# Kernel tuning notes

Measured on AMD Instinct MI355X. Metric: run time of the kernel, lower is better.

Reference implementation:

```python
import jax, jax.numpy as jnp
import numpy as np
from functools import partial

B = 256          # batch_size (== hidden_dim, required by the module's broadcasting)
T = 512          # seq_length
H = 256          # hidden_dim == dim_out
E = 6            # emb_dim
V = 10           # num_input_digits
C = 10           # num_classes


def _kaiming(key, shape):
    fan_in = shape[1]
    return jax.random.normal(key, shape, dtype=jnp.float32) * np.sqrt(2.0 / fan_in)


def setup_inputs() -> dict:
    key = jax.random.key(0)
    ks = jax.random.split(key, 12)
    inp = {
        "x": jax.random.randint(ks[0], (B, T), 0, V),
        "emb": jax.random.normal(ks[1], (V, E), dtype=jnp.float32),
        "Wxg": _kaiming(ks[2], (H, E)), "Whg": _kaiming(ks[3], (H, H)), "bg": jnp.zeros((H,), jnp.float32),
        "Wxi": _kaiming(ks[4], (H, E)), "Whi": _kaiming(ks[5], (H, H)), "bi": jnp.zeros((H,), jnp.float32),
        "Wxf": _kaiming(ks[6], (H, E)), "Whf": _kaiming(ks[7], (H, H)), "bf": jnp.zeros((H,), jnp.float32),
        "Wxo": _kaiming(ks[8], (H, E)), "Who": _kaiming(ks[9], (H, H)), "bo": jnp.zeros((H,), jnp.float32),
        "Wp": _kaiming(ks[10], (C, H)), "bp": jnp.zeros((C,), jnp.float32),
    }
    return inp


def reference(x, emb, Wxg, Whg, bg, Wxi, Whi, bi, Wxf, Whf, bf, Wxo, Who, bo, Wp, bp):
    # x: (B, T) int -> embed -> (B, T, E)
    xe = emb[x]
    # time-major (T, E, B): each step uses x_t.T as in the torch code
    xt_seq = jnp.transpose(xe, (1, 2, 0))

    h0 = jnp.zeros((H, B), jnp.float32)  # h lives as (H, B) per original math
    c0 = jnp.zeros((H, B), jnp.float32)

    def step(carry, xTt):  # xTt: (E, B)
        h, c = carry
        # NOTE: bias (H,) broadcasts over the trailing batch axis (H==B), faithful
        # to the original torch broadcasting.
        g = jnp.tanh(Wxg @ xTt + Whg @ h + bg)
        i = jax.nn.sigmoid(Wxi @ xTt + Whi @ h + bi)
        f = jax.nn.sigmoid(Wxf @ xTt + Whf @ h + bf)
        o = jax.nn.sigmoid(Wxo @ xTt + Who @ h + bo)
        c = g * i + c * f
        h = jnp.tanh(c) * o
        return (h, c), None

    (h, c), _ = jax.lax.scan(step, (h0, c0), xt_seq)
    return (Wp @ h).T + bp  # (B, C)
```

## Files before the change

### kernel.cpp

```cpp
#include <hip/hip_runtime.h>
#include <hip/hip_bf16.h>


typedef __attribute__((ext_vector_type(4))) int   int4v;
typedef __attribute__((ext_vector_type(4))) float float4v;

#define MFMA_I8(a, b, c) __builtin_amdgcn_mfma_i32_16x16x64_i8(a, b, c, 0, 0, 0)

#define K_TANH (-2.8853900817779268f)
#define K_SIG  (-1.4426950408889634f)

#define HSTRIDE 320

__device__ __forceinline__ short f2b(float f) {
    __hip_bfloat16 b = __float2bfloat16(f); return *(short*)&b;
}
__device__ __forceinline__ float b2f(short s) {
    union { unsigned int u; float f; } v; v.u = ((unsigned int)(unsigned short)s) << 16; return v.f;
}
__device__ __forceinline__ float fexp2(float x) {
#if __has_builtin(__builtin_amdgcn_exp2f)
    return __builtin_amdgcn_exp2f(x);
#else
    return __expf(x * 0.6931471805599453f);
#endif
}
__device__ __forceinline__ float frcp(float x) { return __builtin_amdgcn_rcpf(x); }

__global__ __attribute__((amdgpu_flat_work_group_size(1024, 1024), amdgpu_waves_per_eu(4, 4)))
void lstm_i8(
    const int* __restrict__ x,
    const float* __restrict__ emb,
    const float* __restrict__ Wxg, const float* __restrict__ Whg, const float* __restrict__ bg,
    const float* __restrict__ Wxi, const float* __restrict__ Whi, const float* __restrict__ bi,
    const float* __restrict__ Wxf, const float* __restrict__ Whf, const float* __restrict__ bff,
    const float* __restrict__ Wxo, const float* __restrict__ Who, const float* __restrict__ bo,
    const float* __restrict__ Wp, const float* __restrict__ bp,
    float* __restrict__ out)
{
    const int tid = threadIdx.x, bid = blockIdx.x;
    const int c0 = bid * 2;
    const int w = tid >> 6, lane = tid & 63;
    const int l = lane & 15, q = lane >> 4;
    const int col = l & 1;
    const int si  = (l >> 1) & 3;
    const int dup = (l >> 3) & 1;
    const int rw  = 16 * w;
    const int row = rw + 4 * q + si;

    __shared__ __align__(16) unsigned int hbuf[2][2 * HSTRIDE / 4];
    __shared__ __align__(16) short hfin[2 * 264];
    __shared__ unsigned char xdig2[512 * 2];
    __shared__ __align__(16) float tblC[2 * 10 * 1024];
    __shared__ float scaleL[4 * 256];

    const float* WxT[4] = {Wxg, Wxi, Wxf, Wxo};
    const float* WhT[4] = {Whg, Whi, Whf, Who};
    const float* bT[4]  = {bg, bi, bff, bo};

    if (tid < 2 * HSTRIDE / 4) hbuf[0][tid] = 0u;
    if (tid < 1024)
        xdig2[tid] = (unsigned char)x[(c0 + (tid & 1)) * 512 + (tid >> 1)];

    for (int i = tid; i < 5120; i += 1024) {
        int cc  = i / 2560;
        int rem = i - cc * 2560;
        int d = rem >> 8, r = rem & 255;
        float4v v;
        #pragma unroll
        for (int g = 0; g < 4; g++) {
            float s = 0.f;
            #pragma unroll
            for (int e = 0; e < 6; e++) s += WxT[g][r * 6 + e] * emb[d * 6 + e];
            v[g] = (s + bT[g][c0 + cc]) * (g == 0 ? K_TANH : K_SIG);
        }
        *(float4v*)&tblC[cc * 10240 + d * 1024 + r * 4] = v;
    }

    int4v wa[4][4];
    #pragma unroll
    for (int g = 0; g < 4; g++) {
        const float* Wr = WhT[g] + (rw + l) * 256 + q * 16;
        float mx = 0.f;
        #pragma unroll
        for (int kt = 0; kt < 4; kt++)
            #pragma unroll
            for (int c4 = 0; c4 < 4; c4++) {
                float4v v = *(const float4v*)(Wr + kt * 64 + c4 * 4);
                #pragma unroll
                for (int j = 0; j < 4; j++) mx = fmaxf(mx, fabsf(v[j]));
            }
        mx = fmaxf(mx, __shfl_xor(mx, 16));
        mx = fmaxf(mx, __shfl_xor(mx, 32));
        mx = fmaxf(mx, 1e-20f);
        if (q == 0) scaleL[g * 256 + rw + l] = mx;
        float qs = 127.f / mx;
        #pragma unroll
        for (int kt = 0; kt < 4; kt++) {
            int4v f;
            #pragma unroll
            for (int dw = 0; dw < 4; dw++) {
                float4v v = *(const float4v*)(Wr + kt * 64 + dw * 4);
                int word = 0;
                #pragma unroll
                for (int byt = 0; byt < 4; byt++) {
                    int z = (int)rintf(v[byt] * qs);
                    word |= (z & 255) << (8 * byt);
                }
                f[dw] = word;
            }
            wa[g][kt] = f;
        }
    }

    __syncthreads();

    float dscl[4];
    #pragma unroll
    for (int g = 0; g < 4; g++) {
        float kk = (g == 0 ? K_TANH : K_SIG) * (1.f / 16129.f);
        dscl[g] = scaleL[g * 256 + row] * kk;
    }

    const bool bi1 = (si & 1) != 0;
    const bool bi2 = (si & 2) != 0;
    const float* tprow = tblC + col * 10240 + row * 4;
    const int hoff = col * HSTRIDE + row;

    float cs = 0.f, hl = 0.f;

    for (int t = 0; t < 512; t++) {
        const int p = t & 1;
        const char* hbase = (const char*)hbuf[p] + col * HSTRIDE + q * 16;

        int dg = xdig2[t * 2 + col];
        float4v tb = *(const float4v*)(tprow + dg * 1024);

        int4v a0e = {0,0,0,0}, a0o = {0,0,0,0};
        int4v a1e = {0,0,0,0}, a1o = {0,0,0,0};
        int4v a2  = {0,0,0,0}, a3  = {0,0,0,0};
        int4v hf0 = *(const int4v*)(hbase + 0 * 64);
        int4v hf1 = *(const int4v*)(hbase + 1 * 64);
        int4v hf2 = *(const int4v*)(hbase + 2 * 64);
        int4v hf3 = *(const int4v*)(hbase + 3 * 64);
        a0e = MFMA_I8(wa[0][0], hf0, a0e); a0o = MFMA_I8(wa[0][1], hf1, a0o);
        a1e = MFMA_I8(wa[1][0], hf0, a1e); a1o = MFMA_I8(wa[1][1], hf1, a1o);
        a2  = MFMA_I8(wa[2][0], hf0, a2);  a2  = MFMA_I8(wa[2][1], hf1, a2);
        a3  = MFMA_I8(wa[3][0], hf0, a3);  a3  = MFMA_I8(wa[3][1], hf1, a3);
        a0e = MFMA_I8(wa[0][2], hf2, a0e); a0o = MFMA_I8(wa[0][3], hf3, a0o);
        a1e = MFMA_I8(wa[1][2], hf2, a1e); a1o = MFMA_I8(wa[1][3], hf3, a1o);
        a2  = MFMA_I8(wa[2][2], hf2, a2);  a2  = MFMA_I8(wa[2][3], hf3, a2);
        a3  = MFMA_I8(wa[3][2], hf2, a3);  a3  = MFMA_I8(wa[3][3], hf3, a3);
        int4v acc0, acc1;
        #pragma unroll
        for (int i = 0; i < 4; i++) { acc0[i] = a0e[i] + a0o[i]; acc1[i] = a1e[i] + a1o[i]; }

        int av0, av1, av2, av3;
        { int s0 = bi1 ? acc0[1] : acc0[0]; int s1 = bi1 ? acc0[3] : acc0[2]; av0 = bi2 ? s1 : s0; }
        { int s0 = bi1 ? acc1[1] : acc1[0]; int s1 = bi1 ? acc1[3] : acc1[2]; av1 = bi2 ? s1 : s0; }
        { int s0 = bi1 ? a2[1]   : a2[0];   int s1 = bi1 ? a2[3]   : a2[2];   av2 = bi2 ? s1 : s0; }
        { int s0 = bi1 ? a3[1]   : a3[0];   int s1 = bi1 ? a3[3]   : a3[2];   av3 = bi2 ? s1 : s0; }
        {
            float pg = fmaf((float)av0, dscl[0], tb[0]);
            float pi = fmaf((float)av1, dscl[1], tb[1]);
            float pf = fmaf((float)av2, dscl[2], tb[2]);
            float po = fmaf((float)av3, dscl[3], tb[3]);
            float Eg = fexp2(pg), Ei = fexp2(pi), Ef = fexp2(pf), Eo = fexp2(po);
            float m1  = (1.f + Eg) * (1.f + Ei);
            float fp1 = 1.f + Ef;
            float num = fmaf(cs, m1, (1.f - Eg) * fp1);
            float c   = num * frcp(m1 * fp1);
            cs = c;
            float Ec = fexp2(K_TANH * c);
            float hh = (1.f - Ec) * frcp((1.f + Ec) * (1.f + Eo));
            hl = hh;
            if (dup == 0)
                *((char*)hbuf[1 - p] + hoff) = (char)((int)rintf(hh * 127.f));
        }
        __syncthreads();
    }

    if (dup == 0) hfin[col * 264 + row] = f2b(hl);
    __syncthreads();

    if (tid < 20) {
        int pc = tid / 10, cls = tid - pc * 10;
        const short* hcol = &hfin[pc * 264];
        const float* wrow = Wp + cls * 256;
        float s = 0.f;
        #pragma unroll 8
        for (int k = 0; k < 256; k++) s += b2f(hcol[k]) * wrow[k];
        out[(c0 + pc) * 10 + cls] = s + bp[cls];
    }
}

extern "C" void kernel_launch(void* const* d_in, const int* in_sizes, int n_in,
                              void* d_out, int out_size, void* d_ws, size_t ws_size,
                              hipStream_t stream) {
    const int*   x   = (const int*)d_in[0];
    const float* emb = (const float*)d_in[1];
    const float* Wxg = (const float*)d_in[2];
    const float* Whg = (const float*)d_in[3];
    const float* bg  = (const float*)d_in[4];
    const float* Wxi = (const float*)d_in[5];
    const float* Whi = (const float*)d_in[6];
    const float* bi  = (const float*)d_in[7];
    const float* Wxf = (const float*)d_in[8];
    const float* Whf = (const float*)d_in[9];
    const float* bff = (const float*)d_in[10];
    const float* Wxo = (const float*)d_in[11];
    const float* Who = (const float*)d_in[12];
    const float* bo  = (const float*)d_in[13];
    const float* Wp  = (const float*)d_in[14];
    const float* bp  = (const float*)d_in[15];

    hipLaunchKernelGGL(lstm_i8, dim3(128), dim3(1024), 0, stream,
                       x, emb, Wxg, Whg, bg, Wxi, Whi, bi, Wxf, Whf, bff,
                       Wxo, Who, bo, Wp, bp, (float*)d_out);
}
```

Measured before the change: 553.9 us.

## Replace per-step block barrier with LDS flag counters per wave group

The per-timestep __syncthreads is replaced by four shared-memory counters, one per group of four waves. Each group bumps its counter with a workgroup-scope release atomic after writing its slice of h. Each wave waits only on the counter for the h chunk it is about to read, and consumes the four chunks in a rotated order so it starts with data from a different group. MFMA bursts are also wrapped in s_setprio to raise wave priority. This aims to cut barrier stall and let waves overlap across steps, at the cost of spin-polling on volatile LDS and a more delicate ordering argument for reuse of the double buffer.

```diff
diff --git a/kernel.cpp b/kernel.cpp
--- a/kernel.cpp
+++ b/kernel.cpp
@@ -26,6 +26,11 @@
 #endif
 }
 __device__ __forceinline__ float frcp(float x) { return __builtin_amdgcn_rcpf(x); }
+
+__device__ __forceinline__ void spin_ge(volatile int* f, int target) {
+    if (__builtin_expect(*f >= target, 1)) return;
+    while (*f < target) __builtin_amdgcn_s_sleep(1);
+}
 
 __global__ __attribute__((amdgpu_flat_work_group_size(1024, 1024), amdgpu_waves_per_eu(4, 4)))
 void lstm_i8(
@@ -41,6 +46,7 @@
     const int tid = threadIdx.x, bid = blockIdx.x;
     const int c0 = bid * 2;
     const int w = tid >> 6, lane = tid & 63;
+    const int jg = w >> 2;
     const int l = lane & 15, q = lane >> 4;
     const int col = l & 1;
     const int si  = (l >> 1) & 3;
@@ -53,6 +59,7 @@
     __shared__ unsigned char xdig2[512 * 2];
     __shared__ __align__(16) float tblC[2 * 10 * 1024];
     __shared__ float scaleL[4 * 256];
+    __shared__ int wcnt[4];
 
     const float* WxT[4] = {Wxg, Wxi, Wxf, Wxo};
     const float* WhT[4] = {Whg, Whi, Whf, Who};
@@ -61,6 +68,7 @@
     if (tid < 2 * HSTRIDE / 4) hbuf[0][tid] = 0u;
     if (tid < 1024)
         xdig2[tid] = (unsigned char)x[(c0 + (tid & 1)) * 512 + (tid >> 1)];
+    if (tid < 4) wcnt[tid] = 0;
 
     for (int i = tid; i < 5120; i += 1024) {
         int cc  = i / 2560;
@@ -77,7 +85,7 @@
         *(float4v*)&tblC[cc * 10240 + d * 1024 + r * 4] = v;
     }
 
-    int4v wa[4][4];
+    int4v wb[4][4];
     #pragma unroll
     for (int g = 0; g < 4; g++) {
         const float* Wr = WhT[g] + (rw + l) * 256 + q * 16;
@@ -88,7 +96,7 @@
             for (int c4 = 0; c4 < 4; c4++) {
                 float4v v = *(const float4v*)(Wr + kt * 64 + c4 * 4);
                 #pragma unroll
-                for (int j = 0; j < 4; j++) mx = fmaxf(mx, fabsf(v[j]));
+                for (int jj = 0; jj < 4; jj++) mx = fmaxf(mx, fabsf(v[jj]));
             }
         mx = fmaxf(mx, __shfl_xor(mx, 16));
         mx = fmaxf(mx, __shfl_xor(mx, 32));
@@ -96,8 +104,9 @@
         if (q == 0) scaleL[g * 256 + rw + l] = mx;
         float qs = 127.f / mx;
         #pragma unroll
-        for (int kt = 0; kt < 4; kt++) {
-            int4v f;
+        for (int kk = 0; kk < 4; kk++) {
+            const int kt = (jg + 1 + kk) & 3;
+            int4v fr;
             #pragma unroll
             for (int dw = 0; dw < 4; dw++) {
                 float4v v = *(const float4v*)(Wr + kt * 64 + dw * 4);
@@ -107,9 +116,9 @@
                     int z = (int)rintf(v[byt] * qs);
                     word |= (z & 255) << (8 * byt);
                 }
-                f[dw] = word;
+                fr[dw] = word;
             }
-            wa[g][kt] = f;
+            wb[g][kk] = fr;
         }
     }
 
@@ -127,10 +136,18 @@
     const float* tprow = tblC + col * 10240 + row * 4;
     const int hoff = col * HSTRIDE + row;
 
+    const int kts0 = (jg + 1) & 3, kts1 = (jg + 2) & 3, kts2 = (jg + 3) & 3, kts3 = jg;
+    volatile int* fl0 = (volatile int*)&wcnt[kts0];
+    volatile int* fl1 = (volatile int*)&wcnt[kts1];
+    volatile int* fl2 = (volatile int*)&wcnt[kts2];
+    volatile int* fl3 = (volatile int*)&wcnt[kts3];
+    const int ho0 = kts0 * 64, ho1 = kts1 * 64, ho2 = kts2 * 64, ho3 = kts3 * 64;
+
     float cs = 0.f, hl = 0.f;
 
     for (int t = 0; t < 512; t++) {
         const int p = t & 1;
+        const int tt = t << 2;
         const char* hbase = (const char*)hbuf[p] + col * HSTRIDE + q * 16;
 
         int dg = xdig2[t * 2 + col];
@@ -139,18 +156,52 @@
         int4v a0e = {0,0,0,0}, a0o = {0,0,0,0};
         int4v a1e = {0,0,0,0}, a1o = {0,0,0,0};
         int4v a2  = {0,0,0,0}, a3  = {0,0,0,0};
-        int4v hf0 = *(const int4v*)(hbase + 0 * 64);
-        int4v hf1 = *(const int4v*)(hbase + 1 * 64);
-        int4v hf2 = *(const int4v*)(hbase + 2 * 64);
-        int4v hf3 = *(const int4v*)(hbase + 3 * 64);
-        a0e = MFMA_I8(wa[0][0], hf0, a0e); a0o = MFMA_I8(wa[0][1], hf1, a0o);
-        a1e = MFMA_I8(wa[1][0], hf0, a1e); a1o = MFMA_I8(wa[1][1], hf1, a1o);
-        a2  = MFMA_I8(wa[2][0], hf0, a2);  a2  = MFMA_I8(wa[2][1], hf1, a2);
-        a3  = MFMA_I8(wa[3][0], hf0, a3);  a3  = MFMA_I8(wa[3][1], hf1, a3);
-        a0e = MFMA_I8(wa[0][2], hf2, a0e); a0o = MFMA_I8(wa[0][3], hf3, a0o);
-        a1e = MFMA_I8(wa[1][2], hf2, a1e); a1o = MFMA_I8(wa[1][3], hf3, a1o);
-        a2  = MFMA_I8(wa[2][2], hf2, a2);  a2  = MFMA_I8(wa[2][3], hf3, a2);
-        a3  = MFMA_I8(wa[3][2], hf2, a3);  a3  = MFMA_I8(wa[3][3], hf3, a3);
+
+        if (t) spin_ge(fl0, tt);
+        asm volatile("" ::: "memory");
+        {
+            int4v hf = *(const int4v*)(hbase + ho0);
+            __builtin_amdgcn_s_setprio(1);
+            a0e = MFMA_I8(wb[0][0], hf, a0e);
+            a1e = MFMA_I8(wb[1][0], hf, a1e);
+            a2  = MFMA_I8(wb[2][0], hf, a2);
+            a3  = MFMA_I8(wb[3][0], hf, a3);
+            __builtin_amdgcn_s_setprio(0);
+        }
+        if (t) spin_ge(fl1, tt);
+        asm volatile("" ::: "memory");
+        {
+            int4v hf = *(const int4v*)(hbase + ho1);
+            __builtin_amdgcn_s_setprio(1);
+            a0o = MFMA_I8(wb[0][1], hf, a0o);
+            a1o = MFMA_I8(wb[1][1], hf, a1o);
+            a2  = MFMA_I8(wb[2][1], hf, a2);
+            a3  = MFMA_I8(wb[3][1], hf, a3);
+            __builtin_amdgcn_s_setprio(0);
+        }
+        if (t) spin_ge(fl2, tt);
+        asm volatile("" ::: "memory");
+        {
+            int4v hf = *(const int4v*)(hbase + ho2);
+            __builtin_amdgcn_s_setprio(1);
+            a0e = MFMA_I8(wb[0][2], hf, a0e);
+            a1e = MFMA_I8(wb[1][2], hf, a1e);
+            a2  = MFMA_I8(wb[2][2], hf, a2);
+            a3  = MFMA_I8(wb[3][2], hf, a3);
+            __builtin_amdgcn_s_setprio(0);
+        }
+        if (t) spin_ge(fl3, tt);
+        asm volatile("" ::: "memory");
+        {
+            int4v hf = *(const int4v*)(hbase + ho3);
+            __builtin_amdgcn_s_setprio(1);
+            a0o = MFMA_I8(wb[0][3], hf, a0o);
+            a1o = MFMA_I8(wb[1][3], hf, a1o);
+            a2  = MFMA_I8(wb[2][3], hf, a2);
+            a3  = MFMA_I8(wb[3][3], hf, a3);
+            __builtin_amdgcn_s_setprio(0);
+        }
+
         int4v acc0, acc1;
         #pragma unroll
         for (int i = 0; i < 4; i++) { acc0[i] = a0e[i] + a0o[i]; acc1[i] = a1e[i] + a1o[i]; }
@@ -174,10 +225,13 @@
             float Ec = fexp2(K_TANH * c);
             float hh = (1.f - Ec) * frcp((1.f + Ec) * (1.f + Eo));
             hl = hh;
+            if (t == 0 && jg != 0) spin_ge((volatile int*)&wcnt[jg - 1], 4);
             if (dup == 0)
                 *((char*)hbuf[1 - p] + hoff) = (char)((int)rintf(hh * 127.f));
         }
-        __syncthreads();
+        asm volatile("" ::: "memory");
+        if (lane == 0)
+            __hip_atomic_fetch_add(&wcnt[jg], 1, __ATOMIC_RELEASE, __HIP_MEMORY_SCOPE_WORKGROUP);
     }
 
     if (dup == 0) hfin[col * 264 + row] = f2b(hl);
```

New measurement: 698.0 us. +26.0%, slower.

## Halve block to 512 threads with two row tiles per wave and pipelined gate math

Applied to the files above, without the earlier changes.

The block shrinks from 1024 to 512 threads. Each wave now owns two 16-row tiles, so it keeps twice the int8 weight fragments in registers, and the duplicate lanes that previously did redundant work are removed. Inside each timestep, the gate activations for each gate run as soon as that gate's MFMAs finish, and the next step's bias-table lookup is prefetched using precomputed byte offsets. The loop is unrolled by two to fix the ping-pong buffers, and even waves get higher priority. Fewer waves should make each barrier cheaper, at the cost of a longer serial MFMA chain per wave and more register pressure.

```diff
diff --git a/kernel.cpp b/kernel.cpp
--- a/kernel.cpp
+++ b/kernel.cpp
@@ -27,7 +27,7 @@
 }
 __device__ __forceinline__ float frcp(float x) { return __builtin_amdgcn_rcpf(x); }
 
-__global__ __attribute__((amdgpu_flat_work_group_size(1024, 1024), amdgpu_waves_per_eu(4, 4)))
+__global__ __attribute__((amdgpu_flat_work_group_size(512, 512), amdgpu_waves_per_eu(2, 2)))
 void lstm_i8(
     const int* __restrict__ x,
     const float* __restrict__ emb,
@@ -42,15 +42,15 @@
     const int c0 = bid * 2;
     const int w = tid >> 6, lane = tid & 63;
     const int l = lane & 15, q = lane >> 4;
-    const int col = l & 1;
-    const int si  = (l >> 1) & 3;
-    const int dup = (l >> 3) & 1;
-    const int rw  = 16 * w;
-    const int row = rw + 4 * q + si;
+    const int col = lane & 1;
+    const int rtb = (lane >> 1) & 1;
+    const int si  = (lane >> 2) & 3;
+    const int rwb = 32 * w;
+    const int row = rwb + 16 * rtb + 4 * q + si;
 
     __shared__ __align__(16) unsigned int hbuf[2][2 * HSTRIDE / 4];
     __shared__ __align__(16) short hfin[2 * 264];
-    __shared__ unsigned char xdig2[512 * 2];
+    __shared__ __align__(4) unsigned short xoff[2][512];
     __shared__ __align__(16) float tblC[2 * 10 * 1024];
     __shared__ float scaleL[4 * 256];
 
@@ -59,10 +59,12 @@
     const float* bT[4]  = {bg, bi, bff, bo};
 
     if (tid < 2 * HSTRIDE / 4) hbuf[0][tid] = 0u;
-    if (tid < 1024)
-        xdig2[tid] = (unsigned char)x[(c0 + (tid & 1)) * 512 + (tid >> 1)];
-
-    for (int i = tid; i < 5120; i += 1024) {
+    for (int i = tid; i < 1024; i += 512) {
+        int cc = i >> 9, t = i & 511;
+        xoff[cc][t] = (unsigned short)(x[(c0 + cc) * 512 + t] << 12);
+    }
+
+    for (int i = tid; i < 5120; i += 512) {
         int cc  = i / 2560;
         int rem = i - cc * 2560;
         int d = rem >> 8, r = rem & 255;
@@ -77,43 +79,48 @@
         *(float4v*)&tblC[cc * 10240 + d * 1024 + r * 4] = v;
     }
 
-    int4v wa[4][4];
+    int4v wa[2][4][4];
     #pragma unroll
-    for (int g = 0; g < 4; g++) {
-        const float* Wr = WhT[g] + (rw + l) * 256 + q * 16;
-        float mx = 0.f;
+    for (int rt = 0; rt < 2; rt++) {
         #pragma unroll
-        for (int kt = 0; kt < 4; kt++)
+        for (int g = 0; g < 4; g++) {
+            const float* Wr = WhT[g] + (rwb + rt * 16 + l) * 256 + q * 16;
+            float mx = 0.f;
             #pragma unroll
-            for (int c4 = 0; c4 < 4; c4++) {
-                float4v v = *(const float4v*)(Wr + kt * 64 + c4 * 4);
+            for (int kt = 0; kt < 4; kt++)
                 #pragma unroll
-                for (int j = 0; j < 4; j++) mx = fmaxf(mx, fabsf(v[j]));
+                for (int c4 = 0; c4 < 4; c4++) {
+                    float4v v = *(const float4v*)(Wr + kt * 64 + c4 * 4);
+                    #pragma unroll
+                    for (int j = 0; j < 4; j++) mx = fmaxf(mx, fabsf(v[j]));
+                }
+            mx = fmaxf(mx, __shfl_xor(mx, 16));
+            mx = fmaxf(mx, __shfl_xor(mx, 32));
+            mx = fmaxf(mx, 1e-20f);
+            if (q == 0) scaleL[g * 256 + rwb + rt * 16 + l] = mx;
+            float qs = 127.f / mx;
+            #pragma unroll
+            for (int kt = 0; kt < 4; kt++) {
+                int4v f;
+                #pragma unroll
+                for (int dw = 0; dw < 4; dw++) {
+                    float4v v = *(const float4v*)(Wr + kt * 64 + dw * 4);
+                    int word = 0;
+                    #pragma unroll
+                    for (int byt = 0; byt < 4; byt++) {
+                        int z = (int)rintf(v[byt] * qs);
+                        word |= (z & 255) << (8 * byt);
+                    }
+                    f[dw] = word;
+                }
+                wa[rt][g][kt] = f;
             }
-        mx = fmaxf(mx, __shfl_xor(mx, 16));
-        mx = fmaxf(mx, __shfl_xor(mx, 32));
-        mx = fmaxf(mx, 1e-20f);
-        if (q == 0) scaleL[g * 256 + rw + l] = mx;
-        float qs = 127.f / mx;
-        #pragma unroll
-        for (int kt = 0; kt < 4; kt++) {
-            int4v f;
-            #pragma unroll
-            for (int dw = 0; dw < 4; dw++) {
-                float4v v = *(const float4v*)(Wr + kt * 64 + dw * 4);
-                int word = 0;
-                #pragma unroll
-                for (int byt = 0; byt < 4; byt++) {
-                    int z = (int)rintf(v[byt] * qs);
-                    word |= (z & 255) << (8 * byt);
-                }
-                f[dw] = word;
-            }
-            wa[g][kt] = f;
         }
     }
 
     __syncthreads();
+
+    if ((w & 1) == 0) __builtin_amdgcn_s_setprio(1);
 
     float dscl[4];
     #pragma unroll
@@ -124,63 +131,114 @@
 
     const bool bi1 = (si & 1) != 0;
     const bool bi2 = (si & 2) != 0;
-    const float* tprow = tblC + col * 10240 + row * 4;
+    const bool brt = rtb != 0;
+    const char* tprowB = (const char*)(tblC + col * 10240 + row * 4);
     const int hoff = col * HSTRIDE + row;
 
+    const char* hb0 = (const char*)hbuf[0] + col * HSTRIDE + q * 16;
+    const char* hb1 = (const char*)hbuf[1] + col * HSTRIDE + q * 16;
+    char* hw0 = (char*)hbuf[0] + hoff;
+    char* hw1 = (char*)hbuf[1] + hoff;
+    const char* xobase = (const char*)&xoff[col][0];
+
+    const int4v Z = {0, 0, 0, 0};
+
     float cs = 0.f, hl = 0.f;
 
-    for (int t = 0; t < 512; t++) {
-        const int p = t & 1;
-        const char* hbase = (const char*)hbuf[p] + col * HSTRIDE + q * 16;
-
-        int dg = xdig2[t * 2 + col];
-        float4v tb = *(const float4v*)(tprow + dg * 1024);
-
-        int4v a0e = {0,0,0,0}, a0o = {0,0,0,0};
-        int4v a1e = {0,0,0,0}, a1o = {0,0,0,0};
-        int4v a2  = {0,0,0,0}, a3  = {0,0,0,0};
-        int4v hf0 = *(const int4v*)(hbase + 0 * 64);
-        int4v hf1 = *(const int4v*)(hbase + 1 * 64);
-        int4v hf2 = *(const int4v*)(hbase + 2 * 64);
-        int4v hf3 = *(const int4v*)(hbase + 3 * 64);
-        a0e = MFMA_I8(wa[0][0], hf0, a0e); a0o = MFMA_I8(wa[0][1], hf1, a0o);
-        a1e = MFMA_I8(wa[1][0], hf0, a1e); a1o = MFMA_I8(wa[1][1], hf1, a1o);
-        a2  = MFMA_I8(wa[2][0], hf0, a2);  a2  = MFMA_I8(wa[2][1], hf1, a2);
-        a3  = MFMA_I8(wa[3][0], hf0, a3);  a3  = MFMA_I8(wa[3][1], hf1, a3);
-        a0e = MFMA_I8(wa[0][2], hf2, a0e); a0o = MFMA_I8(wa[0][3], hf3, a0o);
-        a1e = MFMA_I8(wa[1][2], hf2, a1e); a1o = MFMA_I8(wa[1][3], hf3, a1o);
-        a2  = MFMA_I8(wa[2][2], hf2, a2);  a2  = MFMA_I8(wa[2][3], hf3, a2);
-        a3  = MFMA_I8(wa[3][2], hf2, a3);  a3  = MFMA_I8(wa[3][3], hf3, a3);
-        int4v acc0, acc1;
-        #pragma unroll
-        for (int i = 0; i < 4; i++) { acc0[i] = a0e[i] + a0o[i]; acc1[i] = a1e[i] + a1o[i]; }
-
-        int av0, av1, av2, av3;
-        { int s0 = bi1 ? acc0[1] : acc0[0]; int s1 = bi1 ? acc0[3] : acc0[2]; av0 = bi2 ? s1 : s0; }
-        { int s0 = bi1 ? acc1[1] : acc1[0]; int s1 = bi1 ? acc1[3] : acc1[2]; av1 = bi2 ? s1 : s0; }
-        { int s0 = bi1 ? a2[1]   : a2[0];   int s1 = bi1 ? a2[3]   : a2[2];   av2 = bi2 ? s1 : s0; }
-        { int s0 = bi1 ? a3[1]   : a3[0];   int s1 = bi1 ? a3[3]   : a3[2];   av3 = bi2 ? s1 : s0; }
-        {
-            float pg = fmaf((float)av0, dscl[0], tb[0]);
-            float pi = fmaf((float)av1, dscl[1], tb[1]);
-            float pf = fmaf((float)av2, dscl[2], tb[2]);
-            float po = fmaf((float)av3, dscl[3], tb[3]);
-            float Eg = fexp2(pg), Ei = fexp2(pi), Ef = fexp2(pf), Eo = fexp2(po);
-            float m1  = (1.f + Eg) * (1.f + Ei);
-            float fp1 = 1.f + Ef;
-            float num = fmaf(cs, m1, (1.f - Eg) * fp1);
-            float c   = num * frcp(m1 * fp1);
-            cs = c;
-            float Ec = fexp2(K_TANH * c);
-            float hh = (1.f - Ec) * frcp((1.f + Ec) * (1.f + Eo));
-            hl = hh;
-            if (dup == 0)
-                *((char*)hbuf[1 - p] + hoff) = (char)((int)rintf(hh * 127.f));
-        }
-        __syncthreads();
-    }
-
-    if (dup == 0) hfin[col * 264 + row] = f2b(hl);
+    unsigned int o01 = *(const unsigned int*)(xobase);
+    float4v tbA = *(const float4v*)(tprowB + (o01 & 0xFFFFu));
+    float4v tbB;
+
+#define SUBSTEP(HB, HW, TBUSE, TBPRE, OFFEXPR)                                              \
+    {                                                                                       \
+        int4v hf0 = *(const int4v*)((HB) + 0 * 64);                                         \
+        int4v hf1 = *(const int4v*)((HB) + 1 * 64);                                         \
+        int4v hf2 = *(const int4v*)((HB) + 2 * 64);                                         \
+        int4v hf3 = *(const int4v*)((HB) + 3 * 64);                                         \
+        int4v ag0 = MFMA_I8(wa[0][0][0], hf0, Z);                                           \
+        int4v ag1 = MFMA_I8(wa[1][0][0], hf0, Z);                                           \
+        int4v ai0 = MFMA_I8(wa[0][1][0], hf0, Z);                                           \
+        int4v ai1 = MFMA_I8(wa[1][1][0], hf0, Z);                                           \
+        int4v af0 = MFMA_I8(wa[0][2][0], hf0, Z);                                           \
+        int4v af1 = MFMA_I8(wa[1][2][0], hf0, Z);                                           \
+        int4v ao0 = MFMA_I8(wa[0][3][0], hf0, Z);                                           \
+        int4v ao1 = MFMA_I8(wa[1][3][0], hf0, Z);                                           \
+        ag0 = MFMA_I8(wa[0][0][1], hf1, ag0);                                               \
+        ag1 = MFMA_I8(wa[1][0][1], hf1, ag1);                                               \
+        ai0 = MFMA_I8(wa[0][1][1], hf1, ai0);                                               \
+        ai1 = MFMA_I8(wa[1][1][1], hf1, ai1);                                               \
+        af0 = MFMA_I8(wa[0][2][1], hf1, af0);                                               \
+        af1 = MFMA_I8(wa[1][2][1], hf1, af1);                                               \
+        ao0 = MFMA_I8(wa[0][3][1], hf1, ao0);                                               \
+        ao1 = MFMA_I8(wa[1][3][1], hf1, ao1);                                               \
+        ag0 = MFMA_I8(wa[0][0][2], hf2, ag0);                                               \
+        ag1 = MFMA_I8(wa[1][0][2], hf2, ag1);                                               \
+        ai0 = MFMA_I8(wa[0][1][2], hf2, ai0);                                               \
+        ai1 = MFMA_I8(wa[1][1][2], hf2, ai1);                                               \
+        af0 = MFMA_I8(wa[0][2][2], hf2, af0);                                               \
+        af1 = MFMA_I8(wa[1][2][2], hf2, af1);                                               \
+        ao0 = MFMA_I8(wa[0][3][2], hf2, ao0);                                               \
+        ao1 = MFMA_I8(wa[1][3][2], hf2, ao1);                                               \
+        TBPRE = *(const float4v*)(tprowB + (OFFEXPR));                                      \
+        ag0 = MFMA_I8(wa[0][0][3], hf3, ag0);                                               \
+        ag1 = MFMA_I8(wa[1][0][3], hf3, ag1);                                               \
+        int avg_;                                                                           \
+        { int t0 = bi1 ? ag0[1] : ag0[0]; int t1 = bi1 ? ag0[3] : ag0[2]; int s0 = bi2 ? t1 : t0; \
+          int u0 = bi1 ? ag1[1] : ag1[0]; int u1 = bi1 ? ag1[3] : ag1[2]; int s1 = bi2 ? u1 : u0; \
+          avg_ = brt ? s1 : s0; }                                                           \
+        float pg = fmaf((float)avg_, dscl[0], (TBUSE)[0]);                                  \
+        float Eg = fexp2(pg);                                                               \
+        ai0 = MFMA_I8(wa[0][1][3], hf3, ai0);                                               \
+        ai1 = MFMA_I8(wa[1][1][3], hf3, ai1);                                               \
+        int avi_;                                                                           \
+        { int t0 = bi1 ? ai0[1] : ai0[0]; int t1 = bi1 ? ai0[3] : ai0[2]; int s0 = bi2 ? t1 : t0; \
+          int u0 = bi1 ? ai1[1] : ai1[0]; int u1 = bi1 ? ai1[3] : ai1[2]; int s1 = bi2 ? u1 : u0; \
+          avi_ = brt ? s1 : s0; }                                                           \
+        float pi = fmaf((float)avi_, dscl[1], (TBUSE)[1]);                                  \
+        float Ei = fexp2(pi);                                                               \
+        float m1 = (1.f + Eg) * (1.f + Ei);                                                 \
+        af0 = MFMA_I8(wa[0][2][3], hf3, af0);                                               \
+        af1 = MFMA_I8(wa[1][2][3], hf3, af1);                                               \
+        int avf_;                                                                           \
+        { int t0 = bi1 ? af0[1] : af0[0]; int t1 = bi1 ? af0[3] : af0[2]; int s0 = bi2 ? t1 : t0; \
+          int u0 = bi1 ? af1[1] : af1[0]; int u1 = bi1 ? af1[3] : af1[2]; int s1 = bi2 ? u1 : u0; \
+          avf_ = brt ? s1 : s0; }                                                           \
+        float pf = fmaf((float)avf_, dscl[2], (TBUSE)[2]);                                  \
+        float Ef = fexp2(pf);                                                               \
+        float fp1 = 1.f + Ef;                                                               \
+        float num = fmaf(cs, m1, (1.f - Eg) * fp1);                                         \
+        float c   = num * frcp(m1 * fp1);                                                   \
+        cs = c;                                                                             \
+        float Ec = fexp2(K_TANH * c);                                                       \
+        ao0 = MFMA_I8(wa[0][3][3], hf3, ao0);                                               \
+        ao1 = MFMA_I8(wa[1][3][3], hf3, ao1);                                               \
+        int avo_;                                                                           \
+        { int t0 = bi1 ? ao0[1] : ao0[0]; int t1 = bi1 ? ao0[3] : ao0[2]; int s0 = bi2 ? t1 : t0; \
+          int u0 = bi1 ? ao1[1] : ao1[0]; int u1 = bi1 ? ao1[3] : ao1[2]; int s1 = bi2 ? u1 : u0; \
+          avo_ = brt ? s1 : s0; }                                                           \
+        float po = fmaf((float)avo_, dscl[3], (TBUSE)[3]);                                  \
+        float Eo = fexp2(po);                                                               \
+        float hh = (1.f - Ec) * frcp((1.f + Ec) * (1.f + Eo));                              \
+        hl = hh;                                                                            \
+        *(HW) = (char)((int)rintf(hh * 127.f));                                             \
+        __syncthreads();                                                                    \
+    }
+
+    for (int i = 0; i < 256; ++i) {
+        const int t2 = i << 1;
+        int tnx = t2 + 2; if (tnx > 510) tnx = 510;
+        unsigned int dn = *(const unsigned int*)(xobase + tnx * 2);
+
+        SUBSTEP(hb0, hw1, tbA, tbB, (o01 >> 16))
+        SUBSTEP(hb1, hw0, tbB, tbA, (dn & 0xFFFFu))
+
+        o01 = dn;
+    }
+#undef SUBSTEP
+
+    if ((w & 1) == 0) __builtin_amdgcn_s_setprio(0);
+
+    hfin[col * 264 + row] = f2b(hl);
     __syncthreads();
 
     if (tid < 20) {
@@ -214,7 +272,7 @@
     const float* Wp  = (const float*)d_in[14];
     const float* bp  = (const float*)d_in[15];
 
-    hipLaunchKernelGGL(lstm_i8, dim3(128), dim3(1024), 0, stream,
+    hipLaunchKernelGGL(lstm_i8, dim3(128), dim3(512), 0, stream,
                        x, emb, Wxg, Whg, bg, Wxi, Whi, bi, Wxf, Whf, bff,
                        Wxo, Who, bo, Wp, bp, (float*)d_out);
 }
```

New measurement: 523.2 us. -5.5%, faster.

## Process four batch columns per block with 512 threads and two interleaved sub-batches

Applied to the files above, without the earlier changes.

Each block now handles four batch columns with 8 waves instead of two columns with 16 waves. Each wave owns 32 hidden rows and holds both row tiles of int8 weights in registers. Two independent column pairs (A and B) are interleaved so that one pair's MFMAs overlap the other's elementwise work. The loop is unrolled by two time steps with prefetched digit offsets, the bias is folded in at use time rather than baked into the table, and s_setprio is applied to alternating waves. This halves the grid to 64 blocks and doubles register pressure, in exchange for fewer waves contending at each barrier and more independent work per wave.

```diff
diff --git a/kernel.cpp b/kernel.cpp
--- a/kernel.cpp
+++ b/kernel.cpp
@@ -10,7 +10,7 @@
 #define K_TANH (-2.8853900817779268f)
 #define K_SIG  (-1.4426950408889634f)
 
-#define HSTRIDE 320
+#define HS 320
 
 __device__ __forceinline__ short f2b(float f) {
     __hip_bfloat16 b = __float2bfloat16(f); return *(short*)&b;
@@ -27,7 +27,7 @@
 }
 __device__ __forceinline__ float frcp(float x) { return __builtin_amdgcn_rcpf(x); }
 
-__global__ __attribute__((amdgpu_flat_work_group_size(1024, 1024), amdgpu_waves_per_eu(4, 4)))
+__global__ __attribute__((amdgpu_flat_work_group_size(512, 512), amdgpu_waves_per_eu(2, 2)))
 void lstm_i8(
     const int* __restrict__ x,
     const float* __restrict__ emb,
@@ -39,81 +39,86 @@
     float* __restrict__ out)
 {
     const int tid = threadIdx.x, bid = blockIdx.x;
-    const int c0 = bid * 2;
+    const int c0 = bid * 4;
     const int w = tid >> 6, lane = tid & 63;
     const int l = lane & 15, q = lane >> 4;
-    const int col = l & 1;
-    const int si  = (l >> 1) & 3;
-    const int dup = (l >> 3) & 1;
-    const int rw  = 16 * w;
-    const int row = rw + 4 * q + si;
-
-    __shared__ __align__(16) unsigned int hbuf[2][2 * HSTRIDE / 4];
-    __shared__ __align__(16) short hfin[2 * 264];
-    __shared__ unsigned char xdig2[512 * 2];
-    __shared__ __align__(16) float tblC[2 * 10 * 1024];
+    const int colb = lane & 1;
+    const int rtb = (lane >> 1) & 1;
+    const int si  = (lane >> 2) & 3;
+    const int rwb = 32 * w;
+    const int row = rwb + 16 * rtb + 4 * q + si;
+
+    __shared__ __align__(16) char hbuf[2][4 * HS];
+    __shared__ __align__(16) short hfin[4 * 264];
+    __shared__ __align__(4) unsigned short xoff[4][512];
+    __shared__ __align__(16) float tblS[10 * 1024];
     __shared__ float scaleL[4 * 256];
 
     const float* WxT[4] = {Wxg, Wxi, Wxf, Wxo};
     const float* WhT[4] = {Whg, Whi, Whf, Who};
     const float* bT[4]  = {bg, bi, bff, bo};
 
-    if (tid < 2 * HSTRIDE / 4) hbuf[0][tid] = 0u;
-    if (tid < 1024)
-        xdig2[tid] = (unsigned char)x[(c0 + (tid & 1)) * 512 + (tid >> 1)];
-
-    for (int i = tid; i < 5120; i += 1024) {
-        int cc  = i / 2560;
-        int rem = i - cc * 2560;
-        int d = rem >> 8, r = rem & 255;
+    if (tid < 4 * HS / 4) ((unsigned int*)hbuf[0])[tid] = 0u;
+    for (int i = tid; i < 2048; i += 512) {
+        int cc = i >> 9, t = i & 511;
+        xoff[cc][t] = (unsigned short)(x[(c0 + cc) * 512 + t] << 12);
+    }
+
+    for (int i = tid; i < 2560; i += 512) {
+        int d = i >> 8, r = i & 255;
         float4v v;
         #pragma unroll
         for (int g = 0; g < 4; g++) {
             float s = 0.f;
             #pragma unroll
             for (int e = 0; e < 6; e++) s += WxT[g][r * 6 + e] * emb[d * 6 + e];
-            v[g] = (s + bT[g][c0 + cc]) * (g == 0 ? K_TANH : K_SIG);
+            v[g] = s;
         }
-        *(float4v*)&tblC[cc * 10240 + d * 1024 + r * 4] = v;
-    }
-
-    int4v wa[4][4];
+        *(float4v*)&tblS[d * 1024 + r * 4] = v;
+    }
+
+    int4v wa[2][4][4];
     #pragma unroll
-    for (int g = 0; g < 4; g++) {
-        const float* Wr = WhT[g] + (rw + l) * 256 + q * 16;
-        float mx = 0.f;
+    for (int rt = 0; rt < 2; rt++) {
         #pragma unroll
-        for (int kt = 0; kt < 4; kt++)
+        for (int g = 0; g < 4; g++) {
+            const float* Wr = WhT[g] + (rwb + rt * 16 + l) * 256 + q * 16;
+            float mx = 0.f;
             #pragma unroll
-            for (int c4 = 0; c4 < 4; c4++) {
-                float4v v = *(const float4v*)(Wr + kt * 64 + c4 * 4);
+            for (int kt = 0; kt < 4; kt++)
                 #pragma unroll
-                for (int j = 0; j < 4; j++) mx = fmaxf(mx, fabsf(v[j]));
+                for (int c4 = 0; c4 < 4; c4++) {
+                    float4v v = *(const float4v*)(Wr + kt * 64 + c4 * 4);
+                    #pragma unroll
+                    for (int j = 0; j < 4; j++) mx = fmaxf(mx, fabsf(v[j]));
+                }
+            mx = fmaxf(mx, __shfl_xor(mx, 16));
+            mx = fmaxf(mx, __shfl_xor(mx, 32));
+            mx = fmaxf(mx, 1e-20f);
+            if (q == 0) scaleL[g * 256 + rwb + rt * 16 + l] = mx;
+            float qs = 127.f / mx;
+            #pragma unroll
+            for (int kt = 0; kt < 4; kt++) {
+                int4v f;
+                #pragma unroll
+                for (int dw = 0; dw < 4; dw++) {
+                    float4v v = *(const float4v*)(Wr + kt * 64 + dw * 4);
+                    int word = 0;
+                    #pragma unroll
+                    for (int byt = 0; byt < 4; byt++) {
+                        int z = (int)rintf(v[byt] * qs);
+                        word |= (z & 255) << (8 * byt);
+                    }
+                    f[dw] = word;
+                }
+                wa[rt][g][kt] = f;
             }
-        mx = fmaxf(mx, __shfl_xor(mx, 16));
-        mx = fmaxf(mx, __shfl_xor(mx, 32));
-        mx = fmaxf(mx, 1e-20f);
-        if (q == 0) scaleL[g * 256 + rw + l] = mx;
-        float qs = 127.f / mx;
-        #pragma unroll
-        for (int kt = 0; kt < 4; kt++) {
-            int4v f;
-            #pragma unroll
-            for (int dw = 0; dw < 4; dw++) {
-                float4v v = *(const float4v*)(Wr + kt * 64 + dw * 4);
-                int word = 0;
-                #pragma unroll
-                for (int byt = 0; byt < 4; byt++) {
-                    int z = (int)rintf(v[byt] * qs);
-                    word |= (z & 255) << (8 * byt);
-                }
-                f[dw] = word;
-            }
-            wa[g][kt] = f;
         }
     }
 
     __syncthreads();
+
+    if ((w & 1) == 0) __builtin_amdgcn_s_setprio(1);
 
     float dscl[4];
     #pragma unroll
@@ -121,69 +126,131 @@
         float kk = (g == 0 ? K_TANH : K_SIG) * (1.f / 16129.f);
         dscl[g] = scaleL[g * 256 + row] * kk;
     }
+    float brvA[4], brvB[4];
+    #pragma unroll
+    for (int g = 0; g < 4; g++) {
+        brvA[g] = bT[g][c0 + colb];
+        brvB[g] = bT[g][c0 + 2 + colb];
+    }
 
     const bool bi1 = (si & 1) != 0;
     const bool bi2 = (si & 2) != 0;
-    const float* tprow = tblC + col * 10240 + row * 4;
-    const int hoff = col * HSTRIDE + row;
-
-    float cs = 0.f, hl = 0.f;
-
-    for (int t = 0; t < 512; t++) {
-        const int p = t & 1;
-        const char* hbase = (const char*)hbuf[p] + col * HSTRIDE + q * 16;
-
-        int dg = xdig2[t * 2 + col];
-        float4v tb = *(const float4v*)(tprow + dg * 1024);
-
-        int4v a0e = {0,0,0,0}, a0o = {0,0,0,0};
-        int4v a1e = {0,0,0,0}, a1o = {0,0,0,0};
-        int4v a2  = {0,0,0,0}, a3  = {0,0,0,0};
-        int4v hf0 = *(const int4v*)(hbase + 0 * 64);
-        int4v hf1 = *(const int4v*)(hbase + 1 * 64);
-        int4v hf2 = *(const int4v*)(hbase + 2 * 64);
-        int4v hf3 = *(const int4v*)(hbase + 3 * 64);
-        a0e = MFMA_I8(wa[0][0], hf0, a0e); a0o = MFMA_I8(wa[0][1], hf1, a0o);
-        a1e = MFMA_I8(wa[1][0], hf0, a1e); a1o = MFMA_I8(wa[1][1], hf1, a1o);
-        a2  = MFMA_I8(wa[2][0], hf0, a2);  a2  = MFMA_I8(wa[2][1], hf1, a2);
-        a3  = MFMA_I8(wa[3][0], hf0, a3);  a3  = MFMA_I8(wa[3][1], hf1, a3);
-        a0e = MFMA_I8(wa[0][2], hf2, a0e); a0o = MFMA_I8(wa[0][3], hf3, a0o);
-        a1e = MFMA_I8(wa[1][2], hf2, a1e); a1o = MFMA_I8(wa[1][3], hf3, a1o);
-        a2  = MFMA_I8(wa[2][2], hf2, a2);  a2  = MFMA_I8(wa[2][3], hf3, a2);
-        a3  = MFMA_I8(wa[3][2], hf2, a3);  a3  = MFMA_I8(wa[3][3], hf3, a3);
-        int4v acc0, acc1;
-        #pragma unroll
-        for (int i = 0; i < 4; i++) { acc0[i] = a0e[i] + a0o[i]; acc1[i] = a1e[i] + a1o[i]; }
-
-        int av0, av1, av2, av3;
-        { int s0 = bi1 ? acc0[1] : acc0[0]; int s1 = bi1 ? acc0[3] : acc0[2]; av0 = bi2 ? s1 : s0; }
-        { int s0 = bi1 ? acc1[1] : acc1[0]; int s1 = bi1 ? acc1[3] : acc1[2]; av1 = bi2 ? s1 : s0; }
-        { int s0 = bi1 ? a2[1]   : a2[0];   int s1 = bi1 ? a2[3]   : a2[2];   av2 = bi2 ? s1 : s0; }
-        { int s0 = bi1 ? a3[1]   : a3[0];   int s1 = bi1 ? a3[3]   : a3[2];   av3 = bi2 ? s1 : s0; }
-        {
-            float pg = fmaf((float)av0, dscl[0], tb[0]);
-            float pi = fmaf((float)av1, dscl[1], tb[1]);
-            float pf = fmaf((float)av2, dscl[2], tb[2]);
-            float po = fmaf((float)av3, dscl[3], tb[3]);
-            float Eg = fexp2(pg), Ei = fexp2(pi), Ef = fexp2(pf), Eo = fexp2(po);
-            float m1  = (1.f + Eg) * (1.f + Ei);
-            float fp1 = 1.f + Ef;
-            float num = fmaf(cs, m1, (1.f - Eg) * fp1);
-            float c   = num * frcp(m1 * fp1);
-            cs = c;
-            float Ec = fexp2(K_TANH * c);
-            float hh = (1.f - Ec) * frcp((1.f + Ec) * (1.f + Eo));
-            hl = hh;
-            if (dup == 0)
-                *((char*)hbuf[1 - p] + hoff) = (char)((int)rintf(hh * 127.f));
-        }
-        __syncthreads();
-    }
-
-    if (dup == 0) hfin[col * 264 + row] = f2b(hl);
+    const bool brt = rtb != 0;
+    const char* tprowB = (const char*)tblS + row * 16;
+
+    const char* rA0 = hbuf[0] + colb * HS + q * 16;
+    const char* rA1 = hbuf[1] + colb * HS + q * 16;
+    const char* rB0 = rA0 + 2 * HS;
+    const char* rB1 = rA1 + 2 * HS;
+    char* wA0 = hbuf[0] + colb * HS + row;
+    char* wA1 = hbuf[1] + colb * HS + row;
+    char* wB0 = wA0 + 2 * HS;
+    char* wB1 = wA1 + 2 * HS;
+    const char* xobA = (const char*)&xoff[colb][0];
+    const char* xobB = (const char*)&xoff[2 + colb][0];
+
+    const int4v Z = {0, 0, 0, 0};
+
+    float csA = 0.f, hlA = 0.f, csB = 0.f, hlB = 0.f;
+
+    unsigned int oA = *(const unsigned int*)(xobA);
+    unsigned int oB = *(const unsigned int*)(xobB);
+
+#define MFMA32(H0, H1, H2, H3, g0, g1, i0, i1, f0, f1, o0, o1)  \
+    g0 = MFMA_I8(wa[0][0][0], H0, Z); g1 = MFMA_I8(wa[1][0][0], H0, Z); \
+    i0 = MFMA_I8(wa[0][1][0], H0, Z); i1 = MFMA_I8(wa[1][1][0], H0, Z); \
+    f0 = MFMA_I8(wa[0][2][0], H0, Z); f1 = MFMA_I8(wa[1][2][0], H0, Z); \
+    o0 = MFMA_I8(wa[0][3][0], H0, Z); o1 = MFMA_I8(wa[1][3][0], H0, Z); \
+    g0 = MFMA_I8(wa[0][0][1], H1, g0); g1 = MFMA_I8(wa[1][0][1], H1, g1); \
+    i0 = MFMA_I8(wa[0][1][1], H1, i0); i1 = MFMA_I8(wa[1][1][1], H1, i1); \
+    f0 = MFMA_I8(wa[0][2][1], H1, f0); f1 = MFMA_I8(wa[1][2][1], H1, f1); \
+    o0 = MFMA_I8(wa[0][3][1], H1, o0); o1 = MFMA_I8(wa[1][3][1], H1, o1); \
+    g0 = MFMA_I8(wa[0][0][2], H2, g0); g1 = MFMA_I8(wa[1][0][2], H2, g1); \
+    i0 = MFMA_I8(wa[0][1][2], H2, i0); i1 = MFMA_I8(wa[1][1][2], H2, i1); \
+    f0 = MFMA_I8(wa[0][2][2], H2, f0); f1 = MFMA_I8(wa[1][2][2], H2, f1); \
+    o0 = MFMA_I8(wa[0][3][2], H2, o0); o1 = MFMA_I8(wa[1][3][2], H2, o1); \
+    g0 = MFMA_I8(wa[0][0][3], H3, g0); g1 = MFMA_I8(wa[1][0][3], H3, g1); \
+    i0 = MFMA_I8(wa[0][1][3], H3, i0); i1 = MFMA_I8(wa[1][1][3], H3, i1); \
+    f0 = MFMA_I8(wa[0][2][3], H3, f0); f1 = MFMA_I8(wa[1][2][3], H3, f1); \
+    o0 = MFMA_I8(wa[0][3][3], H3, o0); o1 = MFMA_I8(wa[1][3][3], H3, o1);
+
+#define ELEM(G0, G1, I0, I1, F0, F1, O0, O1, TS, BRV, CS, HL, WP)  \
+    { \
+        int avg_, avi_, avf_, avo_; \
+        { int t0 = bi1 ? G0[1] : G0[0]; int t1 = bi1 ? G0[3] : G0[2]; int s0 = bi2 ? t1 : t0; \
+          int u0 = bi1 ? G1[1] : G1[0]; int u1 = bi1 ? G1[3] : G1[2]; int s1 = bi2 ? u1 : u0; \
+          avg_ = brt ? s1 : s0; } \
+        { int t0 = bi1 ? I0[1] : I0[0]; int t1 = bi1 ? I0[3] : I0[2]; int s0 = bi2 ? t1 : t0; \
+          int u0 = bi1 ? I1[1] : I1[0]; int u1 = bi1 ? I1[3] : I1[2]; int s1 = bi2 ? u1 : u0; \
+          avi_ = brt ? s1 : s0; } \
+        { int t0 = bi1 ? F0[1] : F0[0]; int t1 = bi1 ? F0[3] : F0[2]; int s0 = bi2 ? t1 : t0; \
+          int u0 = bi1 ? F1[1] : F1[0]; int u1 = bi1 ? F1[3] : F1[2]; int s1 = bi2 ? u1 : u0; \
+          avf_ = brt ? s1 : s0; } \
+        { int t0 = bi1 ? O0[1] : O0[0]; int t1 = bi1 ? O0[3] : O0[2]; int s0 = bi2 ? t1 : t0; \
+          int u0 = bi1 ? O1[1] : O1[0]; int u1 = bi1 ? O1[3] : O1[2]; int s1 = bi2 ? u1 : u0; \
+          avo_ = brt ? s1 : s0; } \
+        float pg = fmaf((float)avg_, dscl[0], (TS[0] + BRV[0]) * K_TANH); \
+        float Eg = fexp2(pg); \
+        float pi = fmaf((float)avi_, dscl[1], (TS[1] + BRV[1]) * K_SIG); \
+        float Ei = fexp2(pi); \
+        float m1 = (1.f + Eg) * (1.f + Ei); \
+        float pf = fmaf((float)avf_, dscl[2], (TS[2] + BRV[2]) * K_SIG); \
+        float Ef = fexp2(pf); \
+        float fp1 = 1.f + Ef; \
+        float num = fmaf(CS, m1, (1.f - Eg) * fp1); \
+        float c = num * frcp(m1 * fp1); \
+        CS = c; \
+        float Ec = fexp2(K_TANH * c); \
+        float po = fmaf((float)avo_, dscl[3], (TS[3] + BRV[3]) * K_SIG); \
+        float Eo = fexp2(po); \
+        float hh = (1.f - Ec) * frcp((1.f + Ec) * (1.f + Eo)); \
+        HL = hh; \
+        *(WP) = (char)((int)rintf(hh * 127.f)); \
+    }
+
+#define SUBD(RA, RB, WA, WB, OFA, OFB, PRE)  \
+    { \
+        int4v hA0 = *(const int4v*)((RA) + 0); \
+        int4v hA1 = *(const int4v*)((RA) + 64); \
+        int4v hA2 = *(const int4v*)((RA) + 128); \
+        int4v hA3 = *(const int4v*)((RA) + 192); \
+        int4v aAg0, aAg1, aAi0, aAi1, aAf0, aAf1, aAo0, aAo1; \
+        MFMA32(hA0, hA1, hA2, hA3, aAg0, aAg1, aAi0, aAi1, aAf0, aAf1, aAo0, aAo1) \
+        int4v hB0 = *(const int4v*)((RB) + 0); \
+        int4v hB1 = *(const int4v*)((RB) + 64); \
+        int4v hB2 = *(const int4v*)((RB) + 128); \
+        int4v hB3 = *(const int4v*)((RB) + 192); \
+        int4v aBg0, aBg1, aBi0, aBi1, aBf0, aBf1, aBo0, aBo1; \
+        MFMA32(hB0, hB1, hB2, hB3, aBg0, aBg1, aBi0, aBi1, aBf0, aBf1, aBo0, aBo1) \
+        float4v tsA = *(const float4v*)(tprowB + (OFA)); \
+        float4v tsB = *(const float4v*)(tprowB + (OFB)); \
+        PRE \
+        ELEM(aAg0, aAg1, aAi0, aAi1, aAf0, aAf1, aAo0, aAo1, tsA, brvA, csA, hlA, WA) \
+        ELEM(aBg0, aBg1, aBi0, aBi1, aBf0, aBf1, aBo0, aBo1, tsB, brvB, csB, hlB, WB) \
+        __syncthreads(); \
+    }
+
+    for (int i = 0; i < 256; ++i) {
+        const int t2 = i << 1;
+        int tnx = t2 + 2; if (tnx > 510) tnx = 510;
+        unsigned int dnA, dnB;
+        SUBD(rA0, rB0, wA1, wB1, (oA & 0xFFFFu), (oB & 0xFFFFu),
+             dnA = *(const unsigned int*)(xobA + tnx * 2);
+             dnB = *(const unsigned int*)(xobB + tnx * 2);)
+        SUBD(rA1, rB1, wA0, wB0, (oA >> 16), (oB >> 16), ;)
+        oA = dnA; oB = dnB;
+    }
+#undef SUBD
+#undef ELEM
+#undef MFMA32
+
+    if ((w & 1) == 0) __builtin_amdgcn_s_setprio(0);
+
+    hfin[colb * 264 + row]       = f2b(hlA);
+    hfin[(2 + colb) * 264 + row] = f2b(hlB);
     __syncthreads();
 
-    if (tid < 20) {
+    if (tid < 40) {
         int pc = tid / 10, cls = tid - pc * 10;
         const short* hcol = &hfin[pc * 264];
         const float* wrow = Wp + cls * 256;
@@ -214,7 +281,7 @@
     const float* Wp  = (const float*)d_in[14];
     const float* bp  = (const float*)d_in[15];
 
-    hipLaunchKernelGGL(lstm_i8, dim3(128), dim3(1024), 0, stream,
+    hipLaunchKernelGGL(lstm_i8, dim3(64), dim3(512), 0, stream,
                        x, emb, Wxg, Whg, bg, Wxi, Whi, bi, Wxf, Whf, bff,
                        Wxo, Who, bo, Wp, bp, (float*)d_out);
 }
```

Result: slower. 864.2 us (+56.0%).
